# Optimization experiments

Hardware: AMD Instinct MI355X
Metric: run time of the kernel (lower is better)

Reference implementation:

```python
import jax, jax.numpy as jnp
import numpy as np


def setup_inputs() -> dict:
    key = jax.random.key(0)
    k1, k2, k3 = jax.random.split(key, 3)
    B, T, D, P = 4, 4096, 512, 4096
    inputs = jax.random.normal(k1, (B, T, D), dtype=jnp.float32)
    # xavier_uniform-like scale for param tokens
    bound = float(np.sqrt(6.0 / (P + D)))
    key_tokens = jax.random.uniform(k2, (P, D), dtype=jnp.float32, minval=-bound, maxval=bound)
    value_tokens = jax.random.uniform(k3, (P, D), dtype=jnp.float32, minval=-bound, maxval=bound)
    return {"inputs": inputs, "key_tokens": key_tokens, "value_tokens": value_tokens}


def reference(inputs, key_tokens, value_tokens):
    # attn_weight: [B, T, P]
    attn = jnp.einsum('btd,pd->btp', inputs, key_tokens)
    # gelu_l2_norm activation: exact GELU, then row-wise L2 norm over param-token dim, scaled by sqrt(P)
    a = jax.nn.gelu(attn, approximate=False)
    scale = jnp.sqrt(jnp.asarray(a.shape[-1], dtype=a.dtype))
    a = a / jnp.linalg.norm(a, axis=-1, keepdims=True) * scale
    # dropout_p = 0.0 -> identity
    return jnp.einsum('btp,pv->btv', a, value_tokens)
```

## Files before the change

### kernel.cpp

```cpp
#include <hip/hip_runtime.h>
#include <hip/hip_bf16.h>


typedef __attribute__((ext_vector_type(8))) short bf16x8;
typedef __attribute__((ext_vector_type(4))) float f32x4;

static constexpr int M_TOTAL = 16384;
static constexpr int DDIM    = 512;
static constexpr int PDIM    = 4096;
static constexpr int BM      = 64;
static constexpr int BP      = 64;
static constexpr int GPAD    = 72;

#define AS1C(p) ((const __attribute__((address_space(1))) void*)(p))
#define AS3(p)  ((__attribute__((address_space(3))) void*)(p))

__device__ __forceinline__ unsigned short f2bf(float f) {
    union { float f; unsigned u; } v; v.f = f;
    unsigned r = v.u + 0x7FFFu + ((v.u >> 16) & 1u);
    return (unsigned short)(r >> 16);
}

__device__ __forceinline__ float gelu_f(float x) {
    float t2 = 2.0f * x * (0.7978845608028654f + 0.035677408136300125f * x * x);
    return x / (1.0f + __expf(-t2));
}

__global__ void conv_k(const float* __restrict__ kin, unsigned short* __restrict__ kbf) {
    int i = (blockIdx.x * 256 + threadIdx.x) * 4;
    float4 v = *reinterpret_cast<const float4*>(kin + i);
    ushort4 o;
    o.x = f2bf(v.x); o.y = f2bf(v.y); o.z = f2bf(v.z); o.w = f2bf(v.w);
    *reinterpret_cast<ushort4*>(kbf + i) = o;
}

__global__ void conv_vt2(const float* __restrict__ vin, unsigned short* __restrict__ vt2) {
    int tid  = blockIdx.x * 256 + threadIdx.x;
    int lane = tid & 63;
    int blk  = tid >> 6;
    int nb = blk & 31;
    int pb = blk >> 5;
    int p0 = pb * 32 + ((lane >> 4) << 3);
    int n  = nb * 16 + (lane & 15);
    ushort4 a, b;
    a.x = f2bf(vin[(p0 + 0) * DDIM + n]);
    a.y = f2bf(vin[(p0 + 1) * DDIM + n]);
    a.z = f2bf(vin[(p0 + 2) * DDIM + n]);
    a.w = f2bf(vin[(p0 + 3) * DDIM + n]);
    b.x = f2bf(vin[(p0 + 4) * DDIM + n]);
    b.y = f2bf(vin[(p0 + 5) * DDIM + n]);
    b.z = f2bf(vin[(p0 + 6) * DDIM + n]);
    b.w = f2bf(vin[(p0 + 7) * DDIM + n]);
    *reinterpret_cast<ushort4*>(vt2 + tid * 8 + 0) = a;
    *reinterpret_cast<ushort4*>(vt2 + tid * 8 + 4) = b;
}

__global__ __launch_bounds__(512, 2) void fused_pattn(
    const float* __restrict__ x,
    const unsigned short* __restrict__ kbf,
    const unsigned short* __restrict__ vt2,
    float* __restrict__ out)
{
    __shared__ unsigned short k_lds[2][BM * DDIM];
    __shared__ unsigned short g_lds[BM * GPAD];
    __shared__ float ss_lds[BM];

    const int tid  = threadIdx.x;
    const int lane = tid & 63;
    const int w    = tid >> 6;
    const int wm   = w >> 1;
    const int wp   = w & 1;
    const int l15  = lane & 15;
    const int l4   = lane >> 4;
    const int m_base = blockIdx.x * BM;

    if (tid < BM) ss_lds[tid] = 0.0f;

    {
        const int P0 = 0;
        #pragma unroll
        for (int i = 0; i < 8; ++i) {
            int r = w * 8 + i;
            const unsigned short* src = kbf + (size_t)(P0 + r) * DDIM + ((lane ^ i) << 3);
            __builtin_amdgcn_global_load_lds(AS1C(src), AS3(&k_lds[0][r * DDIM]), 16, 0, 0);
        }
    }

    bf16x8 xf[16];
    {
        const float* xrow = x + (size_t)(m_base + wm * 16 + l15) * DDIM + l4 * 8;
        #pragma unroll
        for (int db = 0; db < 16; ++db) {
            float4 a = *reinterpret_cast<const float4*>(xrow + db * 32);
            float4 b = *reinterpret_cast<const float4*>(xrow + db * 32 + 4);
            bf16x8 f;
            f[0] = (short)f2bf(a.x); f[1] = (short)f2bf(a.y);
            f[2] = (short)f2bf(a.z); f[3] = (short)f2bf(a.w);
            f[4] = (short)f2bf(b.x); f[5] = (short)f2bf(b.y);
            f[6] = (short)f2bf(b.z); f[7] = (short)f2bf(b.w);
            xf[db] = f;
        }
    }

    f32x4 zero4 = {0.0f, 0.0f, 0.0f, 0.0f};
    f32x4 oacc[4][4];
    #pragma unroll
    for (int i = 0; i < 4; ++i)
        #pragma unroll
        for (int j = 0; j < 4; ++j) oacc[i][j] = zero4;
    float ss = 0.0f;

    int b = 0;
    #pragma unroll 1
    for (int pt = 0; pt < PDIM / BP; ++pt) {
        bf16x8 bg[8];
        {
            const int pb0 = pt * 2;
            #pragma unroll
            for (int ks = 0; ks < 2; ++ks)
                #pragma unroll
                for (int nf = 0; nf < 4; ++nf)
                    bg[ks * 4 + nf] = *reinterpret_cast<const bf16x8*>(
                        vt2 + ((size_t)((pb0 + ks) * 32 + w * 4 + nf) * 64 + lane) * 8);
        }

        {
            const int P0n = ((pt + 1) & 63) * BP;
            #pragma unroll
            for (int i = 0; i < 8; ++i) {
                int r = w * 8 + i;
                const unsigned short* src = kbf + (size_t)(P0n + r) * DDIM + ((lane ^ i) << 3);
                __builtin_amdgcn_global_load_lds(AS1C(src), AS3(&k_lds[b ^ 1][r * DDIM]), 16, 0, 0);
            }
        }

        asm volatile("s_waitcnt vmcnt(16)" ::: "memory");
        __builtin_amdgcn_s_barrier();

        f32x4 sacc[2]; sacc[0] = zero4; sacc[1] = zero4;
        const int swz = (l15 & 7) << 3;
        const unsigned short* kb = &k_lds[b][0];
        __builtin_amdgcn_s_setprio(1);
        #pragma unroll
        for (int db = 0; db < 16; ++db) {
            #pragma unroll
            for (int f = 0; f < 2; ++f) {
                int rowr = wp * 32 + f * 16 + l15;
                int cole = ((db << 5) | (l4 << 3)) ^ swz;
                bf16x8 kv = *reinterpret_cast<const bf16x8*>(kb + rowr * DDIM + cole);
                sacc[f] = __builtin_amdgcn_mfma_f32_16x16x32_bf16(
                    kv, xf[db], sacc[f], 0, 0, 0);
            }
        }
        __builtin_amdgcn_s_setprio(0);

        #pragma unroll
        for (int f = 0; f < 2; ++f) {
            float g0 = gelu_f(sacc[f][0]);
            float g1 = gelu_f(sacc[f][1]);
            float g2 = gelu_f(sacc[f][2]);
            float g3 = gelu_f(sacc[f][3]);
            ss += g0 * g0 + g1 * g1 + g2 * g2 + g3 * g3;
            unsigned d0 = (unsigned)f2bf(g0) | ((unsigned)f2bf(g1) << 16);
            unsigned d1 = (unsigned)f2bf(g2) | ((unsigned)f2bf(g3) << 16);
            int m_l = wm * 16 + l15;
            int p_l = wp * 32 + f * 16 + l4 * 4;
            *reinterpret_cast<uint2*>(&g_lds[m_l * GPAD + p_l]) = make_uint2(d0, d1);
        }
        asm volatile("s_waitcnt lgkmcnt(0)" ::: "memory");
        __builtin_amdgcn_s_barrier();

        __builtin_amdgcn_s_setprio(1);
        #pragma unroll
        for (int ks = 0; ks < 2; ++ks) {
            bf16x8 ag[4];
            #pragma unroll
            for (int mf = 0; mf < 4; ++mf)
                ag[mf] = *reinterpret_cast<const bf16x8*>(
                    &g_lds[(mf * 16 + l15) * GPAD + ks * 32 + l4 * 8]);
            #pragma unroll
            for (int mf = 0; mf < 4; ++mf)
                #pragma unroll
                for (int nf = 0; nf < 4; ++nf)
                    oacc[mf][nf] = __builtin_amdgcn_mfma_f32_16x16x32_bf16(
                        ag[mf], bg[ks * 4 + nf], oacc[mf][nf], 0, 0, 0);
        }
        __builtin_amdgcn_s_setprio(0);

        b ^= 1;
    }

    {
        float v = ss;
        v += __shfl_xor(v, 16, 64);
        v += __shfl_xor(v, 32, 64);
        if (l4 == 0) atomicAdd(&ss_lds[wm * 16 + l15], v);
    }
    __syncthreads();

    #pragma unroll
    for (int mf = 0; mf < 4; ++mf) {
        #pragma unroll
        for (int r = 0; r < 4; ++r) {
            int m_l = mf * 16 + l4 * 4 + r;
            float scale = 64.0f * rsqrtf(ss_lds[m_l]);
            float* orow = out + (size_t)(m_base + m_l) * DDIM + w * 64 + l15;
            #pragma unroll
            for (int nf = 0; nf < 4; ++nf)
                orow[nf * 16] = oacc[mf][nf][r] * scale;
        }
    }
}

extern "C" void kernel_launch(void* const* d_in, const int* in_sizes, int n_in,
                              void* d_out, int out_size, void* d_ws, size_t ws_size,
                              hipStream_t stream) {
    const float* x = (const float*)d_in[0];
    const float* k = (const float*)d_in[1];
    const float* v = (const float*)d_in[2];
    float* out = (float*)d_out;

    unsigned short* kbf = (unsigned short*)d_ws;
    unsigned short* vt2 = kbf + (size_t)PDIM * DDIM;

    conv_k  <<<dim3(2048), dim3(256), 0, stream>>>(k, kbf);
    conv_vt2<<<dim3(1024), dim3(256), 0, stream>>>(v, vt2);
    fused_pattn<<<dim3(M_TOTAL / BM), dim3(512), 0, stream>>>(x, kbf, vt2, out);
}
```

Baseline: 225.6 us.

## Remap first GEMM warp tiling to reuse K fragments across two row blocks

New measurement: 603.5 us. 168% more time.

```diff
diff --git a/kernel.cpp b/kernel.cpp
--- a/kernel.cpp
+++ b/kernel.cpp
@@ -10,7 +10,6 @@
 static constexpr int PDIM    = 4096;
 static constexpr int BM      = 64;
 static constexpr int BP      = 64;
-static constexpr int GPAD    = 72;
 
 #define AS1C(p) ((const __attribute__((address_space(1))) void*)(p))
 #define AS3(p)  ((__attribute__((address_space(3))) void*)(p))
@@ -62,14 +61,14 @@
     float* __restrict__ out)
 {
     __shared__ unsigned short k_lds[2][BM * DDIM];
-    __shared__ unsigned short g_lds[BM * GPAD];
+    __shared__ unsigned short g_lds[BM * BP];
     __shared__ float ss_lds[BM];
 
     const int tid  = threadIdx.x;
     const int lane = tid & 63;
     const int w    = tid >> 6;
-    const int wm   = w >> 1;
-    const int wp   = w & 1;
+    const int mg   = w >> 2;
+    const int pg   = w & 3;
     const int l15  = lane & 15;
     const int l4   = lane >> 4;
     const int m_base = blockIdx.x * BM;
@@ -77,18 +76,18 @@
     if (tid < BM) ss_lds[tid] = 0.0f;
 
     {
-        const int P0 = 0;
         #pragma unroll
         for (int i = 0; i < 8; ++i) {
             int r = w * 8 + i;
-            const unsigned short* src = kbf + (size_t)(P0 + r) * DDIM + ((lane ^ i) << 3);
+            const unsigned short* src = kbf + (size_t)r * DDIM + ((lane ^ i) << 3);
             __builtin_amdgcn_global_load_lds(AS1C(src), AS3(&k_lds[0][r * DDIM]), 16, 0, 0);
         }
     }
 
-    bf16x8 xf[16];
-    {
-        const float* xrow = x + (size_t)(m_base + wm * 16 + l15) * DDIM + l4 * 8;
+    bf16x8 xf[2][16];
+    #pragma unroll
+    for (int mb = 0; mb < 2; ++mb) {
+        const float* xrow = x + (size_t)(m_base + mg * 32 + mb * 16 + l15) * DDIM + l4 * 8;
         #pragma unroll
         for (int db = 0; db < 16; ++db) {
             float4 a = *reinterpret_cast<const float4*>(xrow + db * 32);
@@ -98,7 +97,7 @@
             f[2] = (short)f2bf(a.z); f[3] = (short)f2bf(a.w);
             f[4] = (short)f2bf(b.x); f[5] = (short)f2bf(b.y);
             f[6] = (short)f2bf(b.z); f[7] = (short)f2bf(b.w);
-            xf[db] = f;
+            xf[mb][db] = f;
         }
     }
 
@@ -108,7 +107,7 @@
     for (int i = 0; i < 4; ++i)
         #pragma unroll
         for (int j = 0; j < 4; ++j) oacc[i][j] = zero4;
-    float ss = 0.0f;
+    float ss[2] = {0.0f, 0.0f};
 
     int b = 0;
     #pragma unroll 1
@@ -138,34 +137,32 @@
         __builtin_amdgcn_s_barrier();
 
         f32x4 sacc[2]; sacc[0] = zero4; sacc[1] = zero4;
-        const int swz = (l15 & 7) << 3;
+        const int swz  = (l15 & 7) << 3;
+        const int rowp = pg * 16 + l15;
         const unsigned short* kb = &k_lds[b][0];
         __builtin_amdgcn_s_setprio(1);
         #pragma unroll
         for (int db = 0; db < 16; ++db) {
-            #pragma unroll
-            for (int f = 0; f < 2; ++f) {
-                int rowr = wp * 32 + f * 16 + l15;
-                int cole = ((db << 5) | (l4 << 3)) ^ swz;
-                bf16x8 kv = *reinterpret_cast<const bf16x8*>(kb + rowr * DDIM + cole);
-                sacc[f] = __builtin_amdgcn_mfma_f32_16x16x32_bf16(
-                    kv, xf[db], sacc[f], 0, 0, 0);
-            }
+            int cole = ((db << 5) | (l4 << 3)) ^ swz;
+            bf16x8 kv = *reinterpret_cast<const bf16x8*>(kb + rowp * DDIM + cole);
+            sacc[0] = __builtin_amdgcn_mfma_f32_16x16x32_bf16(kv, xf[0][db], sacc[0], 0, 0, 0);
+            sacc[1] = __builtin_amdgcn_mfma_f32_16x16x32_bf16(kv, xf[1][db], sacc[1], 0, 0, 0);
         }
         __builtin_amdgcn_s_setprio(0);
 
         #pragma unroll
-        for (int f = 0; f < 2; ++f) {
-            float g0 = gelu_f(sacc[f][0]);
-            float g1 = gelu_f(sacc[f][1]);
-            float g2 = gelu_f(sacc[f][2]);
-            float g3 = gelu_f(sacc[f][3]);
-            ss += g0 * g0 + g1 * g1 + g2 * g2 + g3 * g3;
+        for (int mb = 0; mb < 2; ++mb) {
+            float g0 = gelu_f(sacc[mb][0]);
+            float g1 = gelu_f(sacc[mb][1]);
+            float g2 = gelu_f(sacc[mb][2]);
+            float g3 = gelu_f(sacc[mb][3]);
+            ss[mb] += g0 * g0 + g1 * g1 + g2 * g2 + g3 * g3;
             unsigned d0 = (unsigned)f2bf(g0) | ((unsigned)f2bf(g1) << 16);
             unsigned d1 = (unsigned)f2bf(g2) | ((unsigned)f2bf(g3) << 16);
-            int m_l = wm * 16 + l15;
-            int p_l = wp * 32 + f * 16 + l4 * 4;
-            *reinterpret_cast<uint2*>(&g_lds[m_l * GPAD + p_l]) = make_uint2(d0, d1);
+            int m_l   = mg * 32 + mb * 16 + l15;
+            int chunk = (pg << 1) | (l4 >> 1);
+            int elem  = (((chunk ^ (l15 & 7)) << 3) | ((l4 & 1) << 2));
+            *reinterpret_cast<uint2*>(&g_lds[m_l * BP + elem]) = make_uint2(d0, d1);
         }
         asm volatile("s_waitcnt lgkmcnt(0)" ::: "memory");
         __builtin_amdgcn_s_barrier();
@@ -175,9 +172,11 @@
         for (int ks = 0; ks < 2; ++ks) {
             bf16x8 ag[4];
             #pragma unroll
-            for (int mf = 0; mf < 4; ++mf)
+            for (int mf = 0; mf < 4; ++mf) {
+                int chunk = ((ks << 2) | l4) ^ (l15 & 7);
                 ag[mf] = *reinterpret_cast<const bf16x8*>(
-                    &g_lds[(mf * 16 + l15) * GPAD + ks * 32 + l4 * 8]);
+                    &g_lds[(mf * 16 + l15) * BP + (chunk << 3)]);
+            }
             #pragma unroll
             for (int mf = 0; mf < 4; ++mf)
                 #pragma unroll
@@ -190,11 +189,12 @@
         b ^= 1;
     }
 
-    {
-        float v = ss;
+    #pragma unroll
+    for (int mb = 0; mb < 2; ++mb) {
+        float v = ss[mb];
         v += __shfl_xor(v, 16, 64);
         v += __shfl_xor(v, 32, 64);
-        if (l4 == 0) atomicAdd(&ss_lds[wm * 16 + l15], v);
+        if (l4 == 0) atomicAdd(&ss_lds[mg * 32 + mb * 16 + l15], v);
     }
     __syncthreads();
 
```
